# Kernel optimization log

Hardware: AMD Instinct MI355X
Metric: run time of the kernel (lower is better)

Reference implementation:

```python
import jax, jax.numpy as jnp
import numpy as np

N_NODES = 100000
N_EDGES = 1600000
IN_CH = 128
OUT_CH = 128


def setup_inputs() -> dict:
    key = jax.random.key(0)
    k1, k2, k3 = jax.random.split(key, 3)
    x = jax.random.normal(k1, (N_NODES, IN_CH), dtype=jnp.float32)
    edge_index = jax.random.randint(k2, (2, N_EDGES), 0, N_NODES, dtype=jnp.int64)
    # Glorot-style init like PyG GCNConv
    W = jax.random.normal(k3, (IN_CH, OUT_CH), dtype=jnp.float32) * (1.0 / np.sqrt(IN_CH))
    b = jnp.zeros((OUT_CH,), dtype=jnp.float32)
    return {"x": x, "edge_index": edge_index, "W": W, "b": b}


def reference(x, edge_index, W, b):
    N = x.shape[0]
    # add self-loops (PyG GCNConv default add_self_loops=True)
    loop = jnp.arange(N, dtype=edge_index.dtype)
    src = jnp.concatenate([edge_index[0], loop])
    dst = jnp.concatenate([edge_index[1], loop])
    # symmetric normalization: deg computed over destination (col)
    deg = jax.ops.segment_sum(jnp.ones_like(src, dtype=x.dtype), dst, num_segments=N)
    dinv = jnp.where(deg > 0, jax.lax.rsqrt(deg), 0.0)
    norm = dinv[src] * dinv[dst]  # [E+N]
    xw = x @ W  # [N, out_ch]
    msg = xw[src] * norm[:, None]  # gather + scale, [E+N, out_ch]
    out = jax.ops.segment_sum(msg, dst, num_segments=N) + b  # scatter-add
    return jax.nn.relu(out)
```

## Files before the change

### kernel.cpp

```cpp
#include <hip/hip_runtime.h>
#include <hip/hip_bf16.h>

constexpr int CH    = 128;
constexpr int BSH   = 7;
constexpr int CAPSH = 12;
constexpr int CHUNK = 3125;
constexpr int CHCAP = 3200;
constexpr int BKCAP = 2816;

typedef __attribute__((ext_vector_type(8))) short short8v;
typedef __attribute__((ext_vector_type(4))) float f32x4;

__device__ __forceinline__ unsigned short f2bf(float f) {
    unsigned u = __float_as_uint(f);
    u = (u + 0x7fffu + ((u >> 16) & 1u)) >> 16;
    return (unsigned short)u;
}

__global__ __launch_bounds__(256) void k_bin(const int* __restrict__ src,
                                             const int* __restrict__ dst, int E,
                                             int* __restrict__ bucket_cnt,
                                             unsigned* __restrict__ packed,
                                             const float* __restrict__ W,
                                             unsigned short* __restrict__ Wt) {
    __shared__ int hist[1024];
    __shared__ int start[1024];
    __shared__ int cursor[1024];
    __shared__ int gofs[1024];
    __shared__ int tscan[256];
    __shared__ unsigned       sorted[CHCAP];
    __shared__ unsigned short sbkt[CHCAP];

    int t = threadIdx.x;
    if (blockIdx.x < 32) {
        int idx = blockIdx.x * 256 + t;
        int c  = idx & 127;
        int k2 = (idx >> 7) * 2;
        unsigned pk = (unsigned)f2bf(W[(size_t)k2 * CH + c]) |
                      ((unsigned)f2bf(W[(size_t)(k2 + 1) * CH + c]) << 16);
        *(unsigned*)(Wt + (size_t)c * CH + k2) = pk;
    }
    #pragma unroll
    for (int i = 0; i < 4; ++i) hist[t + i * 256] = 0;
    __syncthreads();

    int e0 = blockIdx.x * CHUNK;
    int e1 = min(e0 + CHUNK, E);
    for (int e = e0 + t; e < e1; e += 256)
        atomicAdd(&hist[dst[e] >> BSH], 1);
    __syncthreads();
    int b4 = t * 4;
    int c0 = hist[b4], c1 = hist[b4 + 1], c2 = hist[b4 + 2], c3 = hist[b4 + 3];
    int tsum = c0 + c1 + c2 + c3;
    tscan[t] = tsum;
    __syncthreads();
    for (int off = 1; off < 256; off <<= 1) {
        int v = (t >= off) ? tscan[t - off] : 0;
        __syncthreads();
        tscan[t] += v;
        __syncthreads();
    }
    int eb = tscan[t] - tsum;
    start[b4]     = eb;
    start[b4 + 1] = eb + c0;
    start[b4 + 2] = eb + c0 + c1;
    start[b4 + 3] = eb + c0 + c1 + c2;
    cursor[b4]     = eb;
    cursor[b4 + 1] = eb + c0;
    cursor[b4 + 2] = eb + c0 + c1;
    cursor[b4 + 3] = eb + c0 + c1 + c2;
    __syncthreads();
    #pragma unroll
    for (int i = 0; i < 4; ++i) {
        int b = t + i * 256;
        int c = hist[b];
        gofs[b] = (c > 0) ? atomicAdd(&bucket_cnt[b], c) : 0;
    }
    __syncthreads();
    for (int e = e0 + t; e < e1; e += 256) {
        int d = dst[e];
        int b = d >> BSH;
        int pos = atomicAdd(&cursor[b], 1);
        sorted[pos] = (unsigned)src[e] | ((unsigned)(d & ((1 << BSH) - 1)) << 20);
        sbkt[pos] = (unsigned short)b;
    }
    __syncthreads();
    int nloc = e1 - e0;
    for (int i = t; i < nloc; i += 256) {
        int b = sbkt[i];
        int gpos = (b << CAPSH) + gofs[b] + (i - start[b]);
        packed[gpos] = sorted[i];
    }
}

__global__ __launch_bounds__(256) void k_deg(const int* __restrict__ bucket_cnt,
                                             const unsigned* __restrict__ packed,
                                             float* __restrict__ dinv, int N) {
    __shared__ int fh[128];
    int b = blockIdx.x;
    int t = threadIdx.x;
    int cnt = bucket_cnt[b];
    if (t < 128) fh[t] = 0;
    __syncthreads();
    const unsigned* pk = packed + ((size_t)b << CAPSH);
    for (int i = t; i < cnt; i += 256)
        atomicAdd(&fh[(pk[i] >> 20) & 127], 1);
    __syncthreads();
    if (t < 128) {
        int node = (b << BSH) + t;
        if (node < N) dinv[node] = rsqrtf((float)fh[t] + 1.0f);
    }
}

__global__ __launch_bounds__(256) void k_gemm(const float* __restrict__ x,
                                              const unsigned short* __restrict__ Wt,
                                              const float* __restrict__ dinv,
                                              unsigned short* __restrict__ xwb, int N) {
    __shared__ __align__(16) unsigned short xs[64 * CH];
    int t = threadIdx.x;
    int w = t >> 6, lane = t & 63;
    int c16 = lane & 15, kq = lane >> 4, kb = kq * 8;
    int row0 = blockIdx.x * 64;
    int arow = row0 + w * 16 + c16;
    bool av = arow < N;
    const float* xp = x + (size_t)(av ? arow : 0) * CH;

    f32x4 acc[8];
    #pragma unroll
    for (int f = 0; f < 8; ++f) acc[f] = (f32x4){0.f, 0.f, 0.f, 0.f};

    #pragma unroll
    for (int kc = 0; kc < 4; ++kc) {
        float4 x0 = make_float4(0.f, 0.f, 0.f, 0.f), x1 = x0;
        if (av) {
            x0 = ((const float4*)(xp + kc * 32 + kb))[0];
            x1 = ((const float4*)(xp + kc * 32 + kb))[1];
        }
        union { short8v v; __hip_bfloat162 h[4]; } au;
        au.h[0] = __float22bfloat162_rn(make_float2(x0.x, x0.y));
        au.h[1] = __float22bfloat162_rn(make_float2(x0.z, x0.w));
        au.h[2] = __float22bfloat162_rn(make_float2(x1.x, x1.y));
        au.h[3] = __float22bfloat162_rn(make_float2(x1.z, x1.w));
        #pragma unroll
        for (int f = 0; f < 8; ++f) {
            short8v b = *(const short8v*)(Wt + (size_t)(f * 16 + c16) * CH + kc * 32 + kb);
            acc[f] = __builtin_amdgcn_mfma_f32_16x16x32_bf16(au.v, b, acc[f], 0, 0, 0);
        }
    }

    #pragma unroll
    for (int r = 0; r < 4; ++r) {
        int row_l = w * 16 + kq * 4 + r;
        int grow  = row0 + row_l;
        float dv  = (grow < N) ? dinv[grow] : 0.f;
        #pragma unroll
        for (int f = 0; f < 8; ++f) {
            int col = f * 16 + c16;
            unsigned bo = ((unsigned)((row_l * CH + col) * 2)) ^ ((unsigned)(row_l & 7) << 4);
            *(unsigned short*)((char*)xs + bo) = f2bf(acc[f][r] * dv);
        }
    }
    __syncthreads();
    #pragma unroll
    for (int i = 0; i < 4; ++i) {
        int g = i * 256 + t;
        int row_l = g >> 4;
        unsigned bo = ((unsigned)(g * 16)) ^ ((unsigned)(row_l & 7) << 4);
        uint4 v = *(const uint4*)((const char*)xs + bo);
        int row = row0 + row_l;
        if (row < N) ((uint4*)(xwb + (size_t)row * CH))[g & 15] = v;
    }
}

#define ACC8(U) \
    acc[0] += __uint_as_float((U).x << 16); \
    acc[1] += __uint_as_float((U).x & 0xffff0000u); \
    acc[2] += __uint_as_float((U).y << 16); \
    acc[3] += __uint_as_float((U).y & 0xffff0000u); \
    acc[4] += __uint_as_float((U).z << 16); \
    acc[5] += __uint_as_float((U).z & 0xffff0000u); \
    acc[6] += __uint_as_float((U).w << 16); \
    acc[7] += __uint_as_float((U).w & 0xffff0000u);

__global__ __launch_bounds__(512) void k_gather(const int* __restrict__ bucket_cnt,
                                                const unsigned* __restrict__ packed,
                                                const unsigned short* __restrict__ xwb,
                                                const float* __restrict__ bias,
                                                float* __restrict__ out, int N) {
    __shared__ int fh[128];
    __shared__ int fs[128];
    __shared__ int fc[128];
    __shared__ int elds[BKCAP];
    int b = blockIdx.x;
    int t = threadIdx.x;
    int cnt = min(bucket_cnt[b], BKCAP);
    const unsigned* pk = packed + ((size_t)b << CAPSH);

    if (t < 128) fh[t] = 0;
    __syncthreads();
    for (int i = t; i < cnt; i += 512)
        atomicAdd(&fh[(pk[i] >> 20) & 127], 1);
    __syncthreads();
    if (t < 128) fs[t] = fh[t];
    __syncthreads();
    for (int off = 1; off < 128; off <<= 1) {
        int v = 0;
        if (t < 128 && t >= off) v = fs[t - off];
        __syncthreads();
        if (t < 128) fs[t] += v;
        __syncthreads();
    }
    if (t < 128) fc[t] = fs[t] - fh[t];
    __syncthreads();
    for (int i = t; i < cnt; i += 512) {
        unsigned p = pk[i];
        int f = (p >> 20) & 127;
        int pos = atomicAdd(&fc[f], 1);
        elds[pos] = (int)(p & 0xFFFFF);
    }
    __syncthreads();

    int wv = t >> 6, lane = t & 63;
    int q = lane >> 4, c16 = lane & 15;
    const uint4* xw4 = (const uint4*)xwb;
    for (int i = 0; i < 16; ++i) {
        int nl = wv * 16 + i;
        int n  = (b << BSH) + nl;
        if (n >= N) break;
        int deg = fh[nl];
        int beg = fs[nl] - deg;
        float acc[8];
        #pragma unroll
        for (int k = 0; k < 8; ++k) acc[k] = 0.f;

        for (int p0 = 0; p0 < deg; p0 += 64) {
            int m = deg - p0; if (m > 64) m = 64;
            int myi = 0;
            if (lane < m) myi = elds[beg + p0 + lane];
            int jj = q;
            int a  = __shfl(myi, jj);
            int s  = (jj < m) ? a : N;
            uint4 u = xw4[(size_t)s * 16 + c16];
            for (int j = 4; j < m; j += 4) {
                int jj2 = j + q;
                int ss  = __shfl(myi, jj2 & 63);
                int s2  = (jj2 < m) ? ss : N;
                uint4 u2 = xw4[(size_t)s2 * 16 + c16];
                ACC8(u);
                u = u2;
            }
            ACC8(u);
        }
        #pragma unroll
        for (int k = 0; k < 8; ++k) {
            acc[k] += __shfl_xor(acc[k], 16);
            acc[k] += __shfl_xor(acc[k], 32);
        }
        if (lane < 16) {
            float dn = rsqrtf((float)deg + 1.0f);
            uint4 u = xw4[(size_t)n * 16 + c16];
            ACC8(u);
            float4 b0 = ((const float4*)bias)[c16 * 2];
            float4 b1 = ((const float4*)bias)[c16 * 2 + 1];
            float4 o0, o1;
            o0.x = fmaxf(fmaf(acc[0], dn, b0.x), 0.f);
            o0.y = fmaxf(fmaf(acc[1], dn, b0.y), 0.f);
            o0.z = fmaxf(fmaf(acc[2], dn, b0.z), 0.f);
            o0.w = fmaxf(fmaf(acc[3], dn, b0.w), 0.f);
            o1.x = fmaxf(fmaf(acc[4], dn, b1.x), 0.f);
            o1.y = fmaxf(fmaf(acc[5], dn, b1.y), 0.f);
            o1.z = fmaxf(fmaf(acc[6], dn, b1.z), 0.f);
            o1.w = fmaxf(fmaf(acc[7], dn, b1.w), 0.f);
            ((float4*)(out + (size_t)n * CH))[c16 * 2]     = o0;
            ((float4*)(out + (size_t)n * CH))[c16 * 2 + 1] = o1;
        }
    }
}

extern "C" void kernel_launch(void* const* d_in, const int* in_sizes, int n_in,
                              void* d_out, int out_size, void* d_ws, size_t ws_size,
                              hipStream_t stream) {
    const float* x  = (const float*)d_in[0];
    const int*   ei = (const int*)d_in[1];
    const float* W  = (const float*)d_in[2];
    const float* b  = (const float*)d_in[3];

    int N = in_sizes[0] / CH;
    int E = in_sizes[1] / 2;
    const int* src = ei;
    const int* dst = ei + E;
    float* out = (float*)d_out;

    int nbuck = (N + (1 << BSH) - 1) >> BSH;
    size_t nslots = (size_t)nbuck << CAPSH;

    auto al = [](uintptr_t p) { return (p + 255) & ~(uintptr_t)255; };
    uintptr_t base = (uintptr_t)d_ws;
    unsigned short* xwb = (unsigned short*)base;
    int* bucket_cnt = (int*)(xwb + (size_t)(N + 1) * CH);
    uintptr_t p = al((uintptr_t)(bucket_cnt + nbuck));
    float* dinv     = (float*)p;               p = al(p + (size_t)N * 4);
    unsigned short* Wt = (unsigned short*)p;   p = al(p + (size_t)CH * CH * 2);
    unsigned* packed   = (unsigned*)p;

    int nbin = (E + CHUNK - 1) / CHUNK;

    hipMemsetAsync(xwb + (size_t)N * CH, 0, (size_t)CH * 2 + (size_t)nbuck * 4, stream);
    k_bin   <<<nbin, 256, 0, stream>>>(src, dst, E, bucket_cnt, packed, W, Wt);
    k_deg   <<<nbuck, 256, 0, stream>>>(bucket_cnt, packed, dinv, N);
    k_gemm  <<<(N + 63) / 64, 256, 0, stream>>>(x, Wt, dinv, xwb, N);
    k_gather<<<nbuck, 512, 0, stream>>>(bucket_cnt, packed, xwb, b, out, N);
}
```

Baseline: 150.4 us.

## Fuse degree histogram into GEMM and split gather buckets into halves

Removes the separate degree kernel. Each GEMM block now histograms its own 64 destination nodes from the packed bucket and computes rsqrt of degree inline, so the dinv buffer is gone. The gather kernel launches two blocks per bucket, each handling 64 nodes with a smaller LDS edge list. Both GEMM and gather blocks now scan the full bucket and discard half the entries, which adds redundant reads of the packed list in exchange for one fewer launch and more parallelism in the gather.

```diff
diff --git a/kernel.cpp b/kernel.cpp
--- a/kernel.cpp
+++ b/kernel.cpp
@@ -6,7 +6,7 @@
 constexpr int CAPSH = 12;
 constexpr int CHUNK = 3125;
 constexpr int CHCAP = 3200;
-constexpr int BKCAP = 2816;
+constexpr int HCAP  = 2048;
 
 typedef __attribute__((ext_vector_type(8))) short short8v;
 typedef __attribute__((ext_vector_type(4))) float f32x4;
@@ -93,34 +93,31 @@
     }
 }
 
-__global__ __launch_bounds__(256) void k_deg(const int* __restrict__ bucket_cnt,
-                                             const unsigned* __restrict__ packed,
-                                             float* __restrict__ dinv, int N) {
-    __shared__ int fh[128];
-    int b = blockIdx.x;
-    int t = threadIdx.x;
-    int cnt = bucket_cnt[b];
-    if (t < 128) fh[t] = 0;
-    __syncthreads();
-    const unsigned* pk = packed + ((size_t)b << CAPSH);
-    for (int i = t; i < cnt; i += 256)
-        atomicAdd(&fh[(pk[i] >> 20) & 127], 1);
-    __syncthreads();
-    if (t < 128) {
-        int node = (b << BSH) + t;
-        if (node < N) dinv[node] = rsqrtf((float)fh[t] + 1.0f);
-    }
-}
-
 __global__ __launch_bounds__(256) void k_gemm(const float* __restrict__ x,
                                               const unsigned short* __restrict__ Wt,
-                                              const float* __restrict__ dinv,
+                                              const int* __restrict__ bucket_cnt,
+                                              const unsigned* __restrict__ packed,
                                               unsigned short* __restrict__ xwb, int N) {
+    __shared__ int fh[64];
     __shared__ __align__(16) unsigned short xs[64 * CH];
     int t = threadIdx.x;
     int w = t >> 6, lane = t & 63;
     int c16 = lane & 15, kq = lane >> 4, kb = kq * 8;
     int row0 = blockIdx.x * 64;
+    int bkt  = row0 >> BSH;
+    int half = (row0 >> 6) & 1;
+
+    if (t < 64) fh[t] = 0;
+    __syncthreads();
+    {
+        int cnt = min(bucket_cnt[bkt], 1 << CAPSH);
+        const unsigned* pk = packed + ((size_t)bkt << CAPSH);
+        for (int i = t; i < cnt; i += 256) {
+            int f = (pk[i] >> 20) & 127;
+            if ((f >> 6) == half) atomicAdd(&fh[f & 63], 1);
+        }
+    }
+
     int arow = row0 + w * 16 + c16;
     bool av = arow < N;
     const float* xp = x + (size_t)(av ? arow : 0) * CH;
@@ -148,11 +145,12 @@
         }
     }
 
+    __syncthreads();
     #pragma unroll
     for (int r = 0; r < 4; ++r) {
         int row_l = w * 16 + kq * 4 + r;
         int grow  = row0 + row_l;
-        float dv  = (grow < N) ? dinv[grow] : 0.f;
+        float dv  = (grow < N) ? rsqrtf((float)fh[row_l] + 1.0f) : 0.f;
         #pragma unroll
         for (int f = 0; f < 8; ++f) {
             int col = f * 16 + c16;
@@ -187,45 +185,51 @@
                                                 const unsigned short* __restrict__ xwb,
                                                 const float* __restrict__ bias,
                                                 float* __restrict__ out, int N) {
-    __shared__ int fh[128];
-    __shared__ int fs[128];
-    __shared__ int fc[128];
-    __shared__ int elds[BKCAP];
-    int b = blockIdx.x;
-    int t = threadIdx.x;
-    int cnt = min(bucket_cnt[b], BKCAP);
+    __shared__ int fh[64];
+    __shared__ int fs[64];
+    __shared__ int fc[64];
+    __shared__ int elds[HCAP];
+    int b2 = blockIdx.x;
+    int b  = b2 >> 1;
+    int h  = b2 & 1;
+    int t  = threadIdx.x;
+    int cnt = min(bucket_cnt[b], 1 << CAPSH);
     const unsigned* pk = packed + ((size_t)b << CAPSH);
 
-    if (t < 128) fh[t] = 0;
-    __syncthreads();
-    for (int i = t; i < cnt; i += 512)
-        atomicAdd(&fh[(pk[i] >> 20) & 127], 1);
-    __syncthreads();
-    if (t < 128) fs[t] = fh[t];
-    __syncthreads();
-    for (int off = 1; off < 128; off <<= 1) {
+    if (t < 64) fh[t] = 0;
+    __syncthreads();
+    for (int i = t; i < cnt; i += 512) {
+        int f = (pk[i] >> 20) & 127;
+        if ((f >> 6) == h) atomicAdd(&fh[f & 63], 1);
+    }
+    __syncthreads();
+    if (t < 64) fs[t] = fh[t];
+    __syncthreads();
+    for (int off = 1; off < 64; off <<= 1) {
         int v = 0;
-        if (t < 128 && t >= off) v = fs[t - off];
+        if (t < 64 && t >= off) v = fs[t - off];
         __syncthreads();
-        if (t < 128) fs[t] += v;
+        if (t < 64) fs[t] += v;
         __syncthreads();
     }
-    if (t < 128) fc[t] = fs[t] - fh[t];
+    if (t < 64) fc[t] = fs[t] - fh[t];
     __syncthreads();
     for (int i = t; i < cnt; i += 512) {
         unsigned p = pk[i];
         int f = (p >> 20) & 127;
-        int pos = atomicAdd(&fc[f], 1);
-        elds[pos] = (int)(p & 0xFFFFF);
+        if ((f >> 6) == h) {
+            int pos = atomicAdd(&fc[f & 63], 1);
+            if (pos < HCAP) elds[pos] = (int)(p & 0xFFFFF);
+        }
     }
     __syncthreads();
 
     int wv = t >> 6, lane = t & 63;
     int q = lane >> 4, c16 = lane & 15;
     const uint4* xw4 = (const uint4*)xwb;
-    for (int i = 0; i < 16; ++i) {
-        int nl = wv * 16 + i;
-        int n  = (b << BSH) + nl;
+    for (int i = 0; i < 8; ++i) {
+        int nl = wv * 8 + i;
+        int n  = (b << BSH) + (h << 6) + nl;
         if (n >= N) break;
         int deg = fh[nl];
         int beg = fs[nl] - deg;
@@ -299,7 +303,6 @@
     unsigned short* xwb = (unsigned short*)base;
     int* bucket_cnt = (int*)(xwb + (size_t)(N + 1) * CH);
     uintptr_t p = al((uintptr_t)(bucket_cnt + nbuck));
-    float* dinv     = (float*)p;               p = al(p + (size_t)N * 4);
     unsigned short* Wt = (unsigned short*)p;   p = al(p + (size_t)CH * CH * 2);
     unsigned* packed   = (unsigned*)p;
 
@@ -307,7 +310,6 @@
 
     hipMemsetAsync(xwb + (size_t)N * CH, 0, (size_t)CH * 2 + (size_t)nbuck * 4, stream);
     k_bin   <<<nbin, 256, 0, stream>>>(src, dst, E, bucket_cnt, packed, W, Wt);
-    k_deg   <<<nbuck, 256, 0, stream>>>(bucket_cnt, packed, dinv, N);
-    k_gemm  <<<(N + 63) / 64, 256, 0, stream>>>(x, Wt, dinv, xwb, N);
-    k_gather<<<nbuck, 512, 0, stream>>>(bucket_cnt, packed, xwb, b, out, N);
-}
+    k_gemm  <<<(N + 63) / 64, 256, 0, stream>>>(x, Wt, bucket_cnt, packed, xwb, N);
+    k_gather<<<nbuck * 2, 512, 0, stream>>>(bucket_cnt, packed, xwb, b, out, N);
+}
```

Result: slower. 155.2 us (+3.2%).
